# Performance work log

Hardware: AMD Instinct MI355X
Metric: run time of the kernel (lower is better)

## Reference

```python
import jax, jax.numpy as jnp
import numpy as np

B, N, C = 4, 16384, 512
HEADS = 16
HEADC = C // HEADS
HIDDEN = int(C * 4.0)


def setup_inputs() -> dict:
    key = jax.random.key(0)
    ks = jax.random.split(key, 8)
    s1 = 1.0 / np.sqrt(C)
    s2 = 1.0 / np.sqrt(HIDDEN)
    return {
        "x": jax.random.normal(ks[0], (B, N, C), jnp.float32),
        "mask_matrix": jnp.zeros((1,), jnp.int32),
        "norm1_w": jnp.ones((C,), jnp.float32),
        "norm1_b": jnp.zeros((C,), jnp.float32),
        "kln_w": jnp.ones((HEADS, 1, HEADC), jnp.float32),
        "kln_b": jnp.zeros((HEADS, 1, HEADC), jnp.float32),
        "vln_w": jnp.ones((HEADS, 1, HEADC), jnp.float32),
        "vln_b": jnp.zeros((HEADS, 1, HEADC), jnp.float32),
        "norm2_w": jnp.ones((C,), jnp.float32),
        "norm2_b": jnp.zeros((C,), jnp.float32),
        "fc1_w": jax.random.uniform(ks[1], (HIDDEN, C), jnp.float32, -s1, s1),
        "fc1_b": jax.random.uniform(ks[2], (HIDDEN,), jnp.float32, -s1, s1),
        "fc2_w": jax.random.uniform(ks[3], (C, HIDDEN), jnp.float32, -s2, s2),
        "fc2_b": jax.random.uniform(ks[4], (C,), jnp.float32, -s2, s2),
    }


def _ln(t, w, b, eps=1e-5):
    # standard nn.LayerNorm: biased variance, eps inside sqrt
    mean = t.mean(-1, keepdims=True)
    var = ((t - mean) ** 2).mean(-1, keepdims=True)
    return w * (t - mean) / jnp.sqrt(var + eps) + b


def _ln_std(t, w, b, eps=1e-5):
    # custom LayerNorm: unbiased std (torch.std), eps added to std
    d = t.shape[-1]
    mean = t.mean(-1, keepdims=True)
    var = ((t - mean) ** 2).sum(-1, keepdims=True) / (d - 1)
    return w * ((t - mean) / (jnp.sqrt(var) + eps)) + b


def reference(x, mask_matrix, norm1_w, norm1_b, kln_w, kln_b, vln_w, vln_b,
              norm2_w, norm2_b, fc1_w, fc1_b, fc2_w, fc2_b):
    b, n, c = x.shape
    shortcut = x
    h = _ln(x, norm1_w, norm1_b)
    # simple_attn (softmax-free linear attention)
    qkv = h.reshape(b, n, HEADS, HEADC).transpose(0, 2, 1, 3)  # [B,H,N,D]
    q = qkv
    k = _ln_std(qkv, kln_w, kln_b)
    v = _ln_std(qkv, vln_w, vln_b)
    kv = jnp.einsum('bhnd,bhne->bhde', k, v) / n        # [B,H,D,D]
    attn = jnp.einsum('bhnd,bhde->bhne', q, kv)          # [B,H,N,D]
    attn = attn.transpose(0, 2, 1, 3).reshape(b, n, c)
    h = attn + h                                          # residual inside simple_attn (bias = x post-norm1)
    x = shortcut + h
    # MLP branch
    m = _ln(x, norm2_w, norm2_b)
    m = jax.nn.gelu(m @ fc1_w.T + fc1_b, approximate=False)
    m = m @ fc2_w.T + fc2_b
    return x + m
```

## Files before the change

### kernel.cpp

```cpp
#include <hip/hip_runtime.h>
#include <cstdint>

#define BB 4
#define NN 16384
#define CC 512
#define HH 16
#define DD 32
#define HID 2048
#define MTOT (BB * NN)
#define MCHUNK 16384

typedef __bf16 bf16_t;
typedef __bf16 bf16x8 __attribute__((ext_vector_type(8)));
typedef __bf16 bf16x4 __attribute__((ext_vector_type(4)));
typedef float  f32x4  __attribute__((ext_vector_type(4)));

__device__ __forceinline__ void gload_lds16(const void* g, void* l) {
  auto gp = reinterpret_cast<const __attribute__((address_space(1))) char*>(
      reinterpret_cast<uintptr_t>(g));
  auto lp = reinterpret_cast<__attribute__((address_space(3))) char*>(
      reinterpret_cast<uintptr_t>(l));
  __builtin_amdgcn_global_load_lds(gp, lp, 16, 0, 0);
}

__global__ __launch_bounds__(256) void cvt_bf16_kernel(const float* __restrict__ src,
                                                       bf16_t* __restrict__ dst) {
  const long i = ((long)blockIdx.x * 256 + threadIdx.x) * 4;
  const f32x4 v = *(const f32x4*)(src + i);
  bf16x4 o;
  o[0] = (bf16_t)v[0]; o[1] = (bf16_t)v[1]; o[2] = (bf16_t)v[2]; o[3] = (bf16_t)v[3];
  *(bf16x4*)(dst + i) = o;
}

__global__ __launch_bounds__(256) void norm1_kernel(const float* __restrict__ x,
                                                    const float* __restrict__ w,
                                                    const float* __restrict__ bvec,
                                                    bf16_t* __restrict__ h) {
  const int wv = threadIdx.x >> 6, l = threadIdx.x & 63;
  const long tok = (long)blockIdx.x * 4 + wv;
  const int c0 = l * 8;
  const f32x4 a = *(const f32x4*)(x + tok * CC + c0);
  const f32x4 b = *(const f32x4*)(x + tok * CC + c0 + 4);
  float v[8];
#pragma unroll
  for (int i = 0; i < 4; ++i) { v[i] = a[i]; v[4 + i] = b[i]; }
  float s = 0.f, s2 = 0.f;
#pragma unroll
  for (int i = 0; i < 8; ++i) { s += v[i]; s2 += v[i] * v[i]; }
  for (int off = 32; off; off >>= 1) { s += __shfl_xor(s, off); s2 += __shfl_xor(s2, off); }
  const float mean = s * (1.f / CC);
  const float var  = fmaxf(s2 * (1.f / CC) - mean * mean, 0.f);
  const float rstd = rsqrtf(var + 1e-5f);
  const f32x4 w0 = *(const f32x4*)(w + c0), w1 = *(const f32x4*)(w + c0 + 4);
  const f32x4 b0 = *(const f32x4*)(bvec + c0), b1 = *(const f32x4*)(bvec + c0 + 4);
  bf16x8 o;
#pragma unroll
  for (int i = 0; i < 4; ++i) {
    o[i]     = (bf16_t)(w0[i] * (v[i] - mean) * rstd + b0[i]);
    o[4 + i] = (bf16_t)(w1[i] * (v[4 + i] - mean) * rstd + b1[i]);
  }
  *(bf16x8*)(h + tok * CC + c0) = o;
}

__global__ __launch_bounds__(256) void kv_partial_kernel(const bf16_t* __restrict__ h,
                                                         const float* __restrict__ klw,
                                                         const float* __restrict__ klb,
                                                         const float* __restrict__ vlw,
                                                         const float* __restrict__ vlb,
                                                         float* __restrict__ kvp) {
  __shared__ bf16_t kb[256 * 32];
  __shared__ bf16_t vb[256 * 32];
  __shared__ float scratch[192 * 16];
  const int tid = threadIdx.x;
  const int bh = blockIdx.x >> 6, chunk = blockIdx.x & 63;
  const int head = bh & 15;
  const int b = bh >> 4;
  const long tok0 = ((long)b << 14) + chunk * 256;
  const bf16_t* src = h + (tok0 + tid) * (long)CC + head * DD;
  float hv[32];
  {
    float s = 0.f, s2 = 0.f;
#pragma unroll
    for (int c = 0; c < 4; ++c) {
      const bf16x8 r = *(const bf16x8*)(src + c * 8);
#pragma unroll
      for (int j = 0; j < 8; ++j) {
        hv[c * 8 + j] = (float)r[j]; s += hv[c * 8 + j]; s2 += hv[c * 8 + j] * hv[c * 8 + j];
      }
    }
    const float mean = s * (1.f / 32.f);
    const float varu = fmaxf((s2 - 32.f * mean * mean) * (1.f / 31.f), 0.f);
    const float inv = 1.f / (sqrtf(varu) + 1e-5f);
    const int sx = (tid >> 1) & 3;
#pragma unroll
    for (int c = 0; c < 4; ++c) {
      bf16x8 kc, vc;
#pragma unroll
      for (int j = 0; j < 8; ++j) {
        const int d = c * 8 + j;
        const float t = (hv[d] - mean) * inv;
        kc[j] = (bf16_t)(klw[head * DD + d] * t + klb[head * DD + d]);
        vc[j] = (bf16_t)(vlw[head * DD + d] * t + vlb[head * DD + d]);
      }
      *(bf16x8*)((char*)kb + tid * 64 + ((c ^ sx) * 16)) = kc;
      *(bf16x8*)((char*)vb + tid * 64 + ((c ^ sx) * 16)) = vc;
    }
  }
  __syncthreads();
  const int g = tid >> 6, l = tid & 63;
  const int d0 = (l >> 3) * 4, e0 = (l & 7) * 4;
  const int ck = (l >> 3) >> 1, hk = (l >> 3) & 1;
  const int ce = (l & 7) >> 1, he = l & 1;
  float a[4][4] = {};
  for (int t = g; t < 256; t += 4) {
    const int tx = (t >> 1) & 3;
    const bf16x4 kq = *(const bf16x4*)((const char*)kb + t * 64 + ((ck ^ tx) * 16) + hk * 8);
    const bf16x4 vq = *(const bf16x4*)((const char*)vb + t * 64 + ((ce ^ tx) * 16) + he * 8);
    float kf[4], vf[4];
#pragma unroll
    for (int i2 = 0; i2 < 4; ++i2) { kf[i2] = (float)kq[i2]; vf[i2] = (float)vq[i2]; }
#pragma unroll
    for (int i2 = 0; i2 < 4; ++i2)
#pragma unroll
      for (int j2 = 0; j2 < 4; ++j2) a[i2][j2] += kf[i2] * vf[j2];
  }
  __syncthreads();
  if (g) {
#pragma unroll
    for (int i2 = 0; i2 < 4; ++i2)
#pragma unroll
      for (int j2 = 0; j2 < 4; ++j2)
        scratch[((g - 1) * 64 + l) * 16 + i2 * 4 + j2] = a[i2][j2];
  }
  __syncthreads();
  if (!g) {
#pragma unroll
    for (int gg = 0; gg < 3; ++gg)
#pragma unroll
      for (int i2 = 0; i2 < 4; ++i2)
#pragma unroll
        for (int j2 = 0; j2 < 4; ++j2)
          a[i2][j2] += scratch[(gg * 64 + l) * 16 + i2 * 4 + j2];
    float* dst = kvp + ((long)(bh * 64 + chunk) << 10);
#pragma unroll
    for (int i2 = 0; i2 < 4; ++i2) {
      f32x4 st;
      st[0] = a[i2][0]; st[1] = a[i2][1]; st[2] = a[i2][2]; st[3] = a[i2][3];
      *(f32x4*)&dst[(d0 + i2) * 32 + e0] = st;
    }
  }
}

__global__ __launch_bounds__(256) void kv_reduce_kernel(const float* __restrict__ kvp,
                                                        bf16_t* __restrict__ kvT) {
  const int bh = blockIdx.x;
  const int i4 = threadIdx.x * 4;
  const int d = i4 >> 5, e0 = i4 & 31;
  float s[4] = {};
  const float* p = kvp + ((long)bh << 16) + i4;
  for (int ch = 0; ch < 64; ++ch) {
    const f32x4 t = *(const f32x4*)(p + (ch << 10));
    s[0] += t[0]; s[1] += t[1]; s[2] += t[2]; s[3] += t[3];
  }
  const float sc = 1.f / (float)NN;
  bf16_t* q = kvT + ((long)bh << 10);
#pragma unroll
  for (int j = 0; j < 4; ++j) q[(e0 + j) * 32 + d] = (bf16_t)(s[j] * sc);
}

#define ASTRIDE 520
__global__ __launch_bounds__(256) void attn_fused_kernel(const float* __restrict__ x,
                                                         const bf16_t* __restrict__ h,
                                                         const bf16_t* __restrict__ kvTg,
                                                         const float* __restrict__ n2w,
                                                         const float* __restrict__ n2b,
                                                         float* __restrict__ xout,
                                                         bf16_t* __restrict__ mout) {
  __shared__ bf16_t attn_s[32 * ASTRIDE];
  const int tid = threadIdx.x;
  const int wv = tid >> 6, lane = tid & 63;
  const int lr = lane & 15, kg = lane >> 4;
  const long tok0 = (long)blockIdx.x * 32;
  const int b = (int)(tok0 >> 14);
  const bf16_t* kvsrc = kvTg + ((long)b << 14);

  {
    const int tt = wv & 1, hh = wv >> 1;
    const bf16_t* arow = h + (tok0 + tt * 16 + lr) * (long)CC + kg * 8;
    const f32x4 zero = {};
#pragma unroll
    for (int hi = 0; hi < 8; ++hi) {
      const int hd = hh * 8 + hi;
      const bf16_t* kvh = kvsrc + (hd << 10) + kg * 8;
      const bf16x8 af = *(const bf16x8*)(arow + hd * DD);
      const bf16x8 b0 = *(const bf16x8*)(kvh + lr * 32);
      const bf16x8 b1 = *(const bf16x8*)(kvh + (16 + lr) * 32);
      const f32x4 a0 = __builtin_amdgcn_mfma_f32_16x16x32_bf16(af, b0, zero, 0, 0, 0);
      const f32x4 a1 = __builtin_amdgcn_mfma_f32_16x16x32_bf16(af, b1, zero, 0, 0, 0);
      const int rbase = tt * 16 + kg * 4;
#pragma unroll
      for (int rg = 0; rg < 4; ++rg) {
        attn_s[(rbase + rg) * ASTRIDE + hd * 32 + lr]      = (bf16_t)a0[rg];
        attn_s[(rbase + rg) * ASTRIDE + hd * 32 + 16 + lr] = (bf16_t)a1[rg];
      }
    }
  }
  __syncthreads();

  const int c0 = lane * 8;
  const f32x4 w0 = *(const f32x4*)(n2w + c0), w1 = *(const f32x4*)(n2w + c0 + 4);
  const f32x4 bb0 = *(const f32x4*)(n2b + c0), bb1 = *(const f32x4*)(n2b + c0 + 4);
  for (int it = 0; it < 8; ++it) {
    const int tl = wv * 8 + it;
    const long tok = tok0 + tl;
    const f32x4 xa = *(const f32x4*)(x + tok * CC + c0);
    const f32x4 xb = *(const f32x4*)(x + tok * CC + c0 + 4);
    const bf16x8 hv = *(const bf16x8*)(h + tok * CC + c0);
    const bf16x8 av = *(const bf16x8*)&attn_s[tl * ASTRIDE + c0];
    float x2[8];
#pragma unroll
    for (int i = 0; i < 4; ++i) {
      x2[i]     = xa[i] + (float)hv[i]     + (float)av[i];
      x2[4 + i] = xb[i] + (float)hv[4 + i] + (float)av[4 + i];
    }
    float s = 0.f, s2 = 0.f;
#pragma unroll
    for (int i = 0; i < 8; ++i) { s += x2[i]; s2 += x2[i] * x2[i]; }
    for (int off = 32; off; off >>= 1) { s += __shfl_xor(s, off); s2 += __shfl_xor(s2, off); }
    const float mean = s * (1.f / CC);
    const float var  = fmaxf(s2 * (1.f / CC) - mean * mean, 0.f);
    const float rstd = rsqrtf(var + 1e-5f);
    f32x4 oa, ob;
    bf16x8 om;
#pragma unroll
    for (int i = 0; i < 4; ++i) {
      oa[i] = x2[i]; ob[i] = x2[4 + i];
      om[i]     = (bf16_t)(w0[i] * (x2[i] - mean) * rstd + bb0[i]);
      om[4 + i] = (bf16_t)(w1[i] * (x2[4 + i] - mean) * rstd + bb1[i]);
    }
    *(f32x4*)(xout + tok * CC + c0) = oa;
    *(f32x4*)(xout + tok * CC + c0 + 4) = ob;
    *(bf16x8*)(mout + tok * CC + c0) = om;
  }
}

template <int K, int NOUT, int BN, int WMC, int WNC, bool GELU>
__global__ __launch_bounds__(512, 2) void gemm_kernel(const bf16_t* __restrict__ A,
                                                      const bf16_t* __restrict__ Bw,
                                                      const float* __restrict__ bias,
                                                      bf16_t* __restrict__ outb,
                                                      float* __restrict__ outf) {
  constexpr int ABYTES = 256 * 64;
  constexpr int BBYTES = BN * 64;
  constexpr int BUFB = ABYTES + BBYTES;
  constexpr int LOADS = BUFB / 8192;
  constexpr int MREP = 256 / WMC / 16;
  constexpr int NREP = BN / WNC / 16;
  constexpr int NTILE = NOUT / BN;
  constexpr int NT = K / 32;

  __shared__ bf16_t lds[3 * BUFB / 2];
  const int tid = threadIdx.x;
  const int wid = tid >> 6, lane = tid & 63;
  const int wm = wid / WNC, wn = wid % WNC;
  const int lr = lane & 15, kg = lane >> 4;

  int bid = blockIdx.x;
  const int q = gridDim.x >> 3;
  bid = (bid & 7) * q + (bid >> 3);
  const int bx = bid % NTILE;
  const long by = bid / NTILE;
  const long row0 = by * 256;
  const long col0 = (long)bx * BN;

  const int srow = tid >> 2;
  const int swc = ((tid & 3) ^ ((srow >> 1) & 3)) * 8;
  const bf16_t* gA = A + (row0 + srow) * (long)K + swc;
  const bf16_t* gB = Bw + (col0 + srow) * (long)K + swc;
  char* ldsb = (char*)lds;

#define STAGEK(bufi, kt) do {                                            \
    char* base_ = ldsb + (bufi) * BUFB;                                  \
    gload_lds16(gA + (kt) * 32,            base_ + tid * 16);            \
    gload_lds16(gA + 128L * K + (kt) * 32, base_ + 8192 + tid * 16);     \
    gload_lds16(gB + (kt) * 32,            base_ + ABYTES + tid * 16);   \
    if constexpr (BN == 256)                                             \
      gload_lds16(gB + 128L * K + (kt) * 32,                             \
                  base_ + ABYTES + 8192 + tid * 16);                     \
  } while (0)

  f32x4 acc[MREP][NREP] = {};

  STAGEK(0, 0);
  STAGEK(1, 1);
  if constexpr (LOADS == 4) asm volatile("s_waitcnt vmcnt(4)" ::: "memory");
  else                      asm volatile("s_waitcnt vmcnt(3)" ::: "memory");
  __builtin_amdgcn_s_barrier();

  for (int t = 0; t < NT; ++t) {
    const int cur = t % 3;
    if (t + 2 < NT) STAGEK((t + 2) % 3, t + 2);
    const char* ab = (const char*)ldsb + cur * BUFB;
    const char* bb = ab + ABYTES;
    bf16x8 af[MREP], bf[NREP];
#pragma unroll
    for (int m = 0; m < MREP; ++m) {
      const int row = wm * (256 / WMC) + m * 16 + lr;
      af[m] = *(const bf16x8*)(ab + row * 64 + ((kg ^ ((row >> 1) & 3)) * 16));
    }
#pragma unroll
    for (int n = 0; n < NREP; ++n) {
      const int row = wn * (BN / WNC) + n * 16 + lr;
      bf[n] = *(const bf16x8*)(bb + row * 64 + ((kg ^ ((row >> 1) & 3)) * 16));
    }
    __builtin_amdgcn_s_setprio(1);
#pragma unroll
    for (int m = 0; m < MREP; ++m)
#pragma unroll
      for (int n = 0; n < NREP; ++n)
        acc[m][n] = __builtin_amdgcn_mfma_f32_16x16x32_bf16(af[m], bf[n], acc[m][n], 0, 0, 0);
    __builtin_amdgcn_s_setprio(0);
    if (t + 1 < NT) {
      if (t + 2 < NT) {
        if constexpr (LOADS == 4) asm volatile("s_waitcnt vmcnt(4)" ::: "memory");
        else                      asm volatile("s_waitcnt vmcnt(3)" ::: "memory");
      } else {
        asm volatile("s_waitcnt vmcnt(0)" ::: "memory");
      }
      __builtin_amdgcn_s_barrier();
    }
  }
#undef STAGEK

#pragma unroll
  for (int n = 0; n < NREP; ++n) {
    const long col = col0 + wn * (BN / WNC) + n * 16 + lr;
    const float bs = bias[col];
#pragma unroll
    for (int m = 0; m < MREP; ++m) {
#pragma unroll
      for (int rg = 0; rg < 4; ++rg) {
        const long row = row0 + wm * (256 / WMC) + m * 16 + kg * 4 + rg;
        const float v = acc[m][n][rg] + bs;
        if constexpr (GELU) {
          const float u = 0.7978845608028654f * (v + 0.044715f * v * v * v);
          const float gv = v / (1.f + __expf(-2.f * u));
          outb[row * NOUT + col] = (bf16_t)gv;
        } else {
          outf[row * NOUT + col] += v;
        }
      }
    }
  }
}

extern "C" void kernel_launch(void* const* d_in, const int* in_sizes, int n_in,
                              void* d_out, int out_size, void* d_ws, size_t ws_size,
                              hipStream_t stream) {
  const float* x   = (const float*)d_in[0];
  const float* n1w = (const float*)d_in[2];
  const float* n1b = (const float*)d_in[3];
  const float* klw = (const float*)d_in[4];
  const float* klb = (const float*)d_in[5];
  const float* vlw = (const float*)d_in[6];
  const float* vlb = (const float*)d_in[7];
  const float* n2w = (const float*)d_in[8];
  const float* n2b = (const float*)d_in[9];
  const float* w1f = (const float*)d_in[10];
  const float* b1  = (const float*)d_in[11];
  const float* w2f = (const float*)d_in[12];
  const float* b2  = (const float*)d_in[13];
  float* out = (float*)d_out;

  char* ws = (char*)d_ws;
  bf16_t* h   = (bf16_t*)(ws);
  bf16_t* mb  = (bf16_t*)(ws + (size_t)67108864);
  bf16_t* act = (bf16_t*)(ws + (size_t)134217728);
  bf16_t* w1  = (bf16_t*)(ws + (size_t)201326592);
  bf16_t* w2  = (bf16_t*)(ws + (size_t)203423744);
  float*  kvp = (float*)(ws + (size_t)205520896);
  bf16_t* kvT = (bf16_t*)(ws + (size_t)222298112);

  cvt_bf16_kernel<<<1024, 256, 0, stream>>>(w1f, w1);
  cvt_bf16_kernel<<<1024, 256, 0, stream>>>(w2f, w2);
  norm1_kernel<<<MTOT / 4, 256, 0, stream>>>(x, n1w, n1b, h);
  kv_partial_kernel<<<BB * HH * 64, 256, 0, stream>>>(h, klw, klb, vlw, vlb, kvp);
  kv_reduce_kernel<<<BB * HH, 256, 0, stream>>>(kvp, kvT);
  attn_fused_kernel<<<MTOT / 32, 256, 0, stream>>>(x, h, kvT, n2w, n2b, out, mb);
  for (int ch = 0; ch < MTOT / MCHUNK; ++ch) {
    gemm_kernel<CC, HID, 256, 2, 4, true>
        <<<(MCHUNK / 256) * (HID / 256), 512, 0, stream>>>(
        mb + (long)ch * MCHUNK * CC, w1, b1, act, nullptr);
    gemm_kernel<HID, CC, 128, 4, 2, false>
        <<<(MCHUNK / 256) * (CC / 128), 512, 0, stream>>>(
        act, w2, b2, nullptr, out + (long)ch * MCHUNK * CC);
  }
}
```

Baseline: 633.6 us.

## Rewrite MLP GEMMs as 8-phase ping-pong pipeline with 64-wide K tiles

```diff
diff --git a/kernel.cpp b/kernel.cpp
--- a/kernel.cpp
+++ b/kernel.cpp
@@ -244,104 +244,133 @@
   }
 }
 
-template <int K, int NOUT, int BN, int WMC, int WNC, bool GELU>
-__global__ __launch_bounds__(512, 2) void gemm_kernel(const bf16_t* __restrict__ A,
-                                                      const bf16_t* __restrict__ Bw,
-                                                      const float* __restrict__ bias,
-                                                      bf16_t* __restrict__ outb,
-                                                      float* __restrict__ outf) {
-  constexpr int ABYTES = 256 * 64;
-  constexpr int BBYTES = BN * 64;
-  constexpr int BUFB = ABYTES + BBYTES;
-  constexpr int LOADS = BUFB / 8192;
-  constexpr int MREP = 256 / WMC / 16;
-  constexpr int NREP = BN / WNC / 16;
+template <int K, int NOUT, int BN, bool GELU>
+__global__ __launch_bounds__(512, 2) void gemm8p_kernel(const bf16_t* __restrict__ A,
+                                                        const bf16_t* __restrict__ Bw,
+                                                        const float* __restrict__ bias,
+                                                        bf16_t* __restrict__ outb,
+                                                        float* __restrict__ outf) {
   constexpr int NTILE = NOUT / BN;
-  constexpr int NT = K / 32;
-
-  __shared__ bf16_t lds[3 * BUFB / 2];
+  constexpr int NT = K / 64;
+  constexpr int NI = NT / 2;
+  constexpr int WNSPAN = BN / 4;
+  constexpr int NH = WNSPAN / 32;
+  constexpr int NREP = 2 * NH;
+  constexpr int BLOADS = BN / 128;
+  constexpr int ABYT = 32768;
+  constexpr int BBYT = BN * 128;
+  constexpr int BUFB = ABYT + BBYT;
+  constexpr int WVM = 2 + BLOADS;
+
+  __shared__ char lds[2 * BUFB];
+
   const int tid = threadIdx.x;
   const int wid = tid >> 6, lane = tid & 63;
-  const int wm = wid / WNC, wn = wid % WNC;
+  const int wm = wid >> 2, wn = wid & 3;
   const int lr = lane & 15, kg = lane >> 4;
 
   int bid = blockIdx.x;
-  const int q = gridDim.x >> 3;
-  bid = (bid & 7) * q + (bid >> 3);
-  const int bx = bid % NTILE;
-  const long by = bid / NTILE;
-  const long row0 = by * 256;
-  const long col0 = (long)bx * BN;
+  const int qq = gridDim.x >> 3;
+  bid = (bid & 7) * qq + (bid >> 3);
+  const long row0 = (long)(bid / NTILE) * 256;
+  const long col0 = (long)(bid % NTILE) * BN;
 
   const int srow = tid >> 2;
-  const int swc = ((tid & 3) ^ ((srow >> 1) & 3)) * 8;
-  const bf16_t* gA = A + (row0 + srow) * (long)K + swc;
-  const bf16_t* gB = Bw + (col0 + srow) * (long)K + swc;
-  char* ldsb = (char*)lds;
-
-#define STAGEK(bufi, kt) do {                                            \
-    char* base_ = ldsb + (bufi) * BUFB;                                  \
-    gload_lds16(gA + (kt) * 32,            base_ + tid * 16);            \
-    gload_lds16(gA + 128L * K + (kt) * 32, base_ + 8192 + tid * 16);     \
-    gload_lds16(gB + (kt) * 32,            base_ + ABYTES + tid * 16);   \
-    if constexpr (BN == 256)                                             \
-      gload_lds16(gB + 128L * K + (kt) * 32,                             \
-                  base_ + ABYTES + 8192 + tid * 16);                     \
-  } while (0)
-
-  f32x4 acc[MREP][NREP] = {};
-
-  STAGEK(0, 0);
-  STAGEK(1, 1);
-  if constexpr (LOADS == 4) asm volatile("s_waitcnt vmcnt(4)" ::: "memory");
-  else                      asm volatile("s_waitcnt vmcnt(3)" ::: "memory");
-  __builtin_amdgcn_s_barrier();
-
-  for (int t = 0; t < NT; ++t) {
-    const int cur = t % 3;
-    if (t + 2 < NT) STAGEK((t + 2) % 3, t + 2);
-    const char* ab = (const char*)ldsb + cur * BUFB;
-    const char* bb = ab + ABYTES;
-    bf16x8 af[MREP], bf[NREP];
-#pragma unroll
-    for (int m = 0; m < MREP; ++m) {
-      const int row = wm * (256 / WMC) + m * 16 + lr;
-      af[m] = *(const bf16x8*)(ab + row * 64 + ((kg ^ ((row >> 1) & 3)) * 16));
-    }
-#pragma unroll
-    for (int n = 0; n < NREP; ++n) {
-      const int row = wn * (BN / WNC) + n * 16 + lr;
-      bf[n] = *(const bf16x8*)(bb + row * 64 + ((kg ^ ((row >> 1) & 3)) * 16));
-    }
+  const int sce = (((tid & 3) ^ ((srow >> 1) & 3)) << 3);
+  const bf16_t* pA = A + (row0 + srow) * (long)K + sce;
+  const bf16_t* pB = Bw + (col0 + srow) * (long)K + sce;
+  char* ldsp = (char*)lds;
+
+  auto SA = [&](int buf, int ks, int kt) {
+    char* d_ = ldsp + buf * BUFB + ks * 16384 + tid * 16;
+    const bf16_t* g_ = pA + (long)kt * 64 + ks * 32;
+    gload_lds16(g_, d_);
+    gload_lds16(g_ + 128L * K, d_ + 8192);
+  };
+  auto SB = [&](int buf, int ks, int kt) {
+    char* d_ = ldsp + buf * BUFB + ABYT + ks * (BN * 64) + tid * 16;
+    const bf16_t* g_ = pB + (long)kt * 64 + ks * 32;
+    gload_lds16(g_, d_);
+    if constexpr (BLOADS == 2) gload_lds16(g_ + 128L * K, d_ + 8192);
+  };
+
+  f32x4 acc[8][NREP] = {};
+  bf16x8 af[8], bf[NH];
+
+  auto LDA8 = [&](int buf, int ks) {
+    const char* b_ = ldsp + buf * BUFB + ks * 16384;
+#pragma unroll
+    for (int m = 0; m < 8; ++m) {
+      const int row = wm * 128 + m * 16 + lr;
+      af[m] = *(const bf16x8*)(b_ + row * 64 + ((kg ^ ((row >> 1) & 3)) << 4));
+    }
+  };
+  auto LDBN = [&](int buf, int ks, int nh) {
+    const char* b_ = ldsp + buf * BUFB + ABYT + ks * (BN * 64);
+#pragma unroll
+    for (int n = 0; n < NH; ++n) {
+      const int row = wn * WNSPAN + nh * (WNSPAN / 2) + n * 16 + lr;
+      bf[n] = *(const bf16x8*)(b_ + row * 64 + ((kg ^ ((row >> 1) & 3)) << 4));
+    }
+  };
+  auto MM = [&](int nh) {
     __builtin_amdgcn_s_setprio(1);
 #pragma unroll
-    for (int m = 0; m < MREP; ++m)
-#pragma unroll
-      for (int n = 0; n < NREP; ++n)
-        acc[m][n] = __builtin_amdgcn_mfma_f32_16x16x32_bf16(af[m], bf[n], acc[m][n], 0, 0, 0);
+    for (int m = 0; m < 8; ++m)
+#pragma unroll
+      for (int n = 0; n < NH; ++n)
+        acc[m][nh * NH + n] =
+            __builtin_amdgcn_mfma_f32_16x16x32_bf16(af[m], bf[n], acc[m][nh * NH + n], 0, 0, 0);
     __builtin_amdgcn_s_setprio(0);
-    if (t + 1 < NT) {
-      if (t + 2 < NT) {
-        if constexpr (LOADS == 4) asm volatile("s_waitcnt vmcnt(4)" ::: "memory");
-        else                      asm volatile("s_waitcnt vmcnt(3)" ::: "memory");
-      } else {
-        asm volatile("s_waitcnt vmcnt(0)" ::: "memory");
-      }
-      __builtin_amdgcn_s_barrier();
-    }
-  }
-#undef STAGEK
-
-#pragma unroll
-  for (int n = 0; n < NREP; ++n) {
-    const long col = col0 + wn * (BN / WNC) + n * 16 + lr;
+  };
+  auto WVMW = [&]() {
+    if constexpr (WVM == 4) asm volatile("s_waitcnt vmcnt(4)" ::: "memory");
+    else                    asm volatile("s_waitcnt vmcnt(3)" ::: "memory");
+  };
+#define BARX() __builtin_amdgcn_s_barrier()
+#define LGKM0() asm volatile("s_waitcnt lgkmcnt(0)" ::: "memory")
+
+  SA(0, 0, 0); SA(0, 1, 0); SB(0, 0, 0); SB(0, 1, 0);
+  SA(1, 0, 1); SB(1, 0, 1);
+  WVMW();
+  BARX();
+
+  for (int i = 0; i < NI; ++i) {
+    const int t1 = 2 * i + 1, tA = 2 * i + 2, tB = 2 * i + 3;
+    const bool last = (i == NI - 1);
+    LDA8(0, 0); LDBN(0, 0, 0); SA(1, 1, t1);
+    BARX(); LGKM0(); MM(0); BARX();
+    LDBN(0, 0, 1); SB(1, 1, t1);
+    BARX(); LGKM0(); MM(1); BARX();
+    LDA8(0, 1); LDBN(0, 1, 0); if (tA < NT) SA(0, 0, tA);
+    BARX(); LGKM0(); MM(0); BARX();
+    LDBN(0, 1, 1); if (tA < NT) SB(0, 0, tA);
+    BARX(); LGKM0(); MM(1);
+    if (last) asm volatile("s_waitcnt vmcnt(0)" ::: "memory"); else WVMW();
+    BARX();
+    LDA8(1, 0); LDBN(1, 0, 0); if (tA < NT) SA(0, 1, tA);
+    BARX(); LGKM0(); MM(0); BARX();
+    LDBN(1, 0, 1); if (tA < NT) SB(0, 1, tA);
+    BARX(); LGKM0(); MM(1); BARX();
+    LDA8(1, 1); LDBN(1, 1, 0); if (tB < NT) SA(1, 0, tB);
+    BARX(); LGKM0(); MM(0); BARX();
+    LDBN(1, 1, 1); if (tB < NT) SB(1, 0, tB);
+    BARX(); LGKM0(); MM(1);
+    if (!last) { WVMW(); BARX(); }
+  }
+#undef BARX
+#undef LGKM0
+
+#pragma unroll
+  for (int j = 0; j < NREP; ++j) {
+    const long col = col0 + wn * WNSPAN + j * 16 + lr;
     const float bs = bias[col];
 #pragma unroll
-    for (int m = 0; m < MREP; ++m) {
+    for (int m = 0; m < 8; ++m) {
 #pragma unroll
       for (int rg = 0; rg < 4; ++rg) {
-        const long row = row0 + wm * (256 / WMC) + m * 16 + kg * 4 + rg;
-        const float v = acc[m][n][rg] + bs;
+        const long row = row0 + wm * 128 + m * 16 + kg * 4 + rg;
+        const float v = acc[m][j][rg] + bs;
         if constexpr (GELU) {
           const float u = 0.7978845608028654f * (v + 0.044715f * v * v * v);
           const float gv = v / (1.f + __expf(-2.f * u));
@@ -388,10 +417,10 @@
   kv_reduce_kernel<<<BB * HH, 256, 0, stream>>>(kvp, kvT);
   attn_fused_kernel<<<MTOT / 32, 256, 0, stream>>>(x, h, kvT, n2w, n2b, out, mb);
   for (int ch = 0; ch < MTOT / MCHUNK; ++ch) {
-    gemm_kernel<CC, HID, 256, 2, 4, true>
+    gemm8p_kernel<CC, HID, 256, true>
         <<<(MCHUNK / 256) * (HID / 256), 512, 0, stream>>>(
         mb + (long)ch * MCHUNK * CC, w1, b1, act, nullptr);
-    gemm_kernel<HID, CC, 128, 4, 2, false>
+    gemm8p_kernel<HID, CC, 128, false>
         <<<(MCHUNK / 256) * (CC / 128), 512, 0, stream>>>(
         act, w2, b2, nullptr, out + (long)ch * MCHUNK * CC);
   }
```

Result: no change. 638.9 us (+0.8%).

## Replace triple-buffered 256-row GEMM with simple 128x128 single-buffer tiles and LDS-staged GELU stores

Applied to the files above, without the earlier changes.

```diff
diff --git a/kernel.cpp b/kernel.cpp
--- a/kernel.cpp
+++ b/kernel.cpp
@@ -8,7 +8,6 @@
 #define DD 32
 #define HID 2048
 #define MTOT (BB * NN)
-#define MCHUNK 16384
 
 typedef __bf16 bf16_t;
 typedef __bf16 bf16x8 __attribute__((ext_vector_type(8)));
@@ -244,110 +243,98 @@
   }
 }
 
-template <int K, int NOUT, int BN, int WMC, int WNC, bool GELU>
-__global__ __launch_bounds__(512, 2) void gemm_kernel(const bf16_t* __restrict__ A,
-                                                      const bf16_t* __restrict__ Bw,
-                                                      const float* __restrict__ bias,
-                                                      bf16_t* __restrict__ outb,
-                                                      float* __restrict__ outf) {
-  constexpr int ABYTES = 256 * 64;
-  constexpr int BBYTES = BN * 64;
-  constexpr int BUFB = ABYTES + BBYTES;
-  constexpr int LOADS = BUFB / 8192;
-  constexpr int MREP = 256 / WMC / 16;
-  constexpr int NREP = BN / WNC / 16;
-  constexpr int NTILE = NOUT / BN;
+template <int K, int NOUT, bool GELU>
+__global__ __launch_bounds__(256, 3) void gemm97_kernel(const bf16_t* __restrict__ A,
+                                                        const bf16_t* __restrict__ Bw,
+                                                        const float* __restrict__ bias,
+                                                        bf16_t* __restrict__ outb,
+                                                        float* __restrict__ outf) {
+  constexpr int NTILE = NOUT / 128;
   constexpr int NT = K / 32;
-
-  __shared__ bf16_t lds[3 * BUFB / 2];
+  __shared__ char lds[32768];
+  char* As = lds;
+  char* Bs = lds + 8192;
+
   const int tid = threadIdx.x;
   const int wid = tid >> 6, lane = tid & 63;
-  const int wm = wid / WNC, wn = wid % WNC;
+  const int wr = wid >> 1, wc = wid & 1;
   const int lr = lane & 15, kg = lane >> 4;
 
   int bid = blockIdx.x;
-  const int q = gridDim.x >> 3;
-  bid = (bid & 7) * q + (bid >> 3);
-  const int bx = bid % NTILE;
-  const long by = bid / NTILE;
-  const long row0 = by * 256;
-  const long col0 = (long)bx * BN;
+  const int qq = gridDim.x >> 3;
+  bid = (bid & 7) * qq + (bid >> 3);
+  const long row0 = (long)(bid / NTILE) * 128;
+  const long col0 = (long)(bid % NTILE) * 128;
 
   const int srow = tid >> 2;
-  const int swc = ((tid & 3) ^ ((srow >> 1) & 3)) * 8;
-  const bf16_t* gA = A + (row0 + srow) * (long)K + swc;
-  const bf16_t* gB = Bw + (col0 + srow) * (long)K + swc;
-  char* ldsb = (char*)lds;
-
-#define STAGEK(bufi, kt) do {                                            \
-    char* base_ = ldsb + (bufi) * BUFB;                                  \
-    gload_lds16(gA + (kt) * 32,            base_ + tid * 16);            \
-    gload_lds16(gA + 128L * K + (kt) * 32, base_ + 8192 + tid * 16);     \
-    gload_lds16(gB + (kt) * 32,            base_ + ABYTES + tid * 16);   \
-    if constexpr (BN == 256)                                             \
-      gload_lds16(gB + 128L * K + (kt) * 32,                             \
-                  base_ + ABYTES + 8192 + tid * 16);                     \
-  } while (0)
-
-  f32x4 acc[MREP][NREP] = {};
-
-  STAGEK(0, 0);
-  STAGEK(1, 1);
-  if constexpr (LOADS == 4) asm volatile("s_waitcnt vmcnt(4)" ::: "memory");
-  else                      asm volatile("s_waitcnt vmcnt(3)" ::: "memory");
-  __builtin_amdgcn_s_barrier();
-
-  for (int t = 0; t < NT; ++t) {
-    const int cur = t % 3;
-    if (t + 2 < NT) STAGEK((t + 2) % 3, t + 2);
-    const char* ab = (const char*)ldsb + cur * BUFB;
-    const char* bb = ab + ABYTES;
-    bf16x8 af[MREP], bf[NREP];
-#pragma unroll
-    for (int m = 0; m < MREP; ++m) {
-      const int row = wm * (256 / WMC) + m * 16 + lr;
-      af[m] = *(const bf16x8*)(ab + row * 64 + ((kg ^ ((row >> 1) & 3)) * 16));
-    }
-#pragma unroll
-    for (int n = 0; n < NREP; ++n) {
-      const int row = wn * (BN / WNC) + n * 16 + lr;
-      bf[n] = *(const bf16x8*)(bb + row * 64 + ((kg ^ ((row >> 1) & 3)) * 16));
-    }
-    __builtin_amdgcn_s_setprio(1);
-#pragma unroll
-    for (int m = 0; m < MREP; ++m)
-#pragma unroll
-      for (int n = 0; n < NREP; ++n)
+  const int sce = (((tid & 3) ^ ((srow >> 1) & 3)) << 3);
+  const bf16_t* gA = A + (row0 + srow) * (long)K + sce;
+  const bf16_t* gB = Bw + (col0 + srow) * (long)K + sce;
+
+  f32x4 acc[4][4] = {};
+
+  const int cx = ((kg ^ ((lr >> 1) & 3)) << 4);
+  const char* aB = As + (wr * 64 + lr) * 64 + cx;
+  const char* bB = Bs + (wc * 64 + lr) * 64 + cx;
+
+  for (int kt = 0; kt < NT; ++kt) {
+    gload_lds16(gA + kt * 32, As + tid * 16);
+    gload_lds16(gA + 64L * K + kt * 32, As + 4096 + tid * 16);
+    gload_lds16(gB + kt * 32, Bs + tid * 16);
+    gload_lds16(gB + 64L * K + kt * 32, Bs + 4096 + tid * 16);
+    __syncthreads();
+    bf16x8 af[4], bf[4];
+#pragma unroll
+    for (int m = 0; m < 4; ++m) af[m] = *(const bf16x8*)(aB + m * 1024);
+#pragma unroll
+    for (int n = 0; n < 4; ++n) bf[n] = *(const bf16x8*)(bB + n * 1024);
+#pragma unroll
+    for (int m = 0; m < 4; ++m)
+#pragma unroll
+      for (int n = 0; n < 4; ++n)
         acc[m][n] = __builtin_amdgcn_mfma_f32_16x16x32_bf16(af[m], bf[n], acc[m][n], 0, 0, 0);
-    __builtin_amdgcn_s_setprio(0);
-    if (t + 1 < NT) {
-      if (t + 2 < NT) {
-        if constexpr (LOADS == 4) asm volatile("s_waitcnt vmcnt(4)" ::: "memory");
-        else                      asm volatile("s_waitcnt vmcnt(3)" ::: "memory");
-      } else {
-        asm volatile("s_waitcnt vmcnt(0)" ::: "memory");
-      }
-      __builtin_amdgcn_s_barrier();
-    }
-  }
-#undef STAGEK
-
-#pragma unroll
-  for (int n = 0; n < NREP; ++n) {
-    const long col = col0 + wn * (BN / WNC) + n * 16 + lr;
-    const float bs = bias[col];
-#pragma unroll
-    for (int m = 0; m < MREP; ++m) {
-#pragma unroll
-      for (int rg = 0; rg < 4; ++rg) {
-        const long row = row0 + wm * (256 / WMC) + m * 16 + kg * 4 + rg;
-        const float v = acc[m][n][rg] + bs;
-        if constexpr (GELU) {
+    __syncthreads();
+  }
+
+  if constexpr (GELU) {
+    bf16_t* ot = (bf16_t*)lds;
+#pragma unroll
+    for (int n = 0; n < 4; ++n) {
+      const int col = wc * 64 + n * 16 + lr;
+      const float bs = bias[col0 + col];
+#pragma unroll
+      for (int m = 0; m < 4; ++m) {
+#pragma unroll
+        for (int rg = 0; rg < 4; ++rg) {
+          const int row = wr * 64 + m * 16 + kg * 4 + rg;
+          const float v = acc[m][n][rg] + bs;
           const float u = 0.7978845608028654f * (v + 0.044715f * v * v * v);
           const float gv = v / (1.f + __expf(-2.f * u));
-          outb[row * NOUT + col] = (bf16_t)gv;
-        } else {
-          outf[row * NOUT + col] += v;
+          const int ch = (col >> 3) ^ ((row >> 2) & 3);
+          ot[row * 128 + ch * 8 + (col & 7)] = (bf16_t)gv;
+        }
+      }
+    }
+    __syncthreads();
+#pragma unroll
+    for (int it2 = 0; it2 < 8; ++it2) {
+      const int idx = it2 * 256 + tid;
+      const int row = idx >> 4, ch = idx & 15;
+      const int chs = ch ^ ((row >> 2) & 3);
+      const bf16x8 vv = *(const bf16x8*)&ot[row * 128 + chs * 8];
+      *(bf16x8*)(outb + (row0 + row) * NOUT + col0 + ch * 8) = vv;
+    }
+  } else {
+#pragma unroll
+    for (int n = 0; n < 4; ++n) {
+      const long col = col0 + wc * 64 + n * 16 + lr;
+      const float bs = bias[col];
+#pragma unroll
+      for (int m = 0; m < 4; ++m) {
+#pragma unroll
+        for (int rg = 0; rg < 4; ++rg) {
+          const long row = row0 + wr * 64 + m * 16 + kg * 4 + rg;
+          outf[row * NOUT + col] += acc[m][n][rg] + bs;
         }
       }
     }
@@ -372,14 +359,20 @@
   const float* b2  = (const float*)d_in[13];
   float* out = (float*)d_out;
 
+  int nch;
+  if (ws_size >= 289538048ULL) nch = 2;
+  else                         nch = 4;
+  const long mch = MTOT / nch;
+
   char* ws = (char*)d_ws;
-  bf16_t* h   = (bf16_t*)(ws);
-  bf16_t* mb  = (bf16_t*)(ws + (size_t)67108864);
-  bf16_t* act = (bf16_t*)(ws + (size_t)134217728);
-  bf16_t* w1  = (bf16_t*)(ws + (size_t)201326592);
-  bf16_t* w2  = (bf16_t*)(ws + (size_t)203423744);
-  float*  kvp = (float*)(ws + (size_t)205520896);
-  bf16_t* kvT = (bf16_t*)(ws + (size_t)222298112);
+  size_t off = 0;
+  bf16_t* h   = (bf16_t*)(ws + off); off += (size_t)MTOT * CC * 2;
+  bf16_t* mb  = (bf16_t*)(ws + off); off += (size_t)MTOT * CC * 2;
+  bf16_t* act = (bf16_t*)(ws + off); off += (size_t)mch * HID * 2;
+  bf16_t* w1  = (bf16_t*)(ws + off); off += (size_t)HID * CC * 2;
+  bf16_t* w2  = (bf16_t*)(ws + off); off += (size_t)HID * CC * 2;
+  float*  kvp = (float*)(ws + off);  off += (size_t)BB * HH * 64 * 1024 * 4;
+  bf16_t* kvT = (bf16_t*)(ws + off);
 
   cvt_bf16_kernel<<<1024, 256, 0, stream>>>(w1f, w1);
   cvt_bf16_kernel<<<1024, 256, 0, stream>>>(w2f, w2);
@@ -387,12 +380,12 @@
   kv_partial_kernel<<<BB * HH * 64, 256, 0, stream>>>(h, klw, klb, vlw, vlb, kvp);
   kv_reduce_kernel<<<BB * HH, 256, 0, stream>>>(kvp, kvT);
   attn_fused_kernel<<<MTOT / 32, 256, 0, stream>>>(x, h, kvT, n2w, n2b, out, mb);
-  for (int ch = 0; ch < MTOT / MCHUNK; ++ch) {
-    gemm_kernel<CC, HID, 256, 2, 4, true>
-        <<<(MCHUNK / 256) * (HID / 256), 512, 0, stream>>>(
-        mb + (long)ch * MCHUNK * CC, w1, b1, act, nullptr);
-    gemm_kernel<HID, CC, 128, 4, 2, false>
-        <<<(MCHUNK / 256) * (CC / 128), 512, 0, stream>>>(
-        act, w2, b2, nullptr, out + (long)ch * MCHUNK * CC);
-  }
-}
+  for (int ch = 0; ch < nch; ++ch) {
+    gemm97_kernel<CC, HID, true>
+        <<<(int)((mch / 128) * (HID / 128)), 256, 0, stream>>>(
+        mb + (size_t)ch * mch * CC, w1, b1, act, nullptr);
+    gemm97_kernel<HID, CC, false>
+        <<<(int)((mch / 128) * (CC / 128)), 256, 0, stream>>>(
+        act, w2, b2, nullptr, out + (size_t)ch * mch * CC);
+  }
+}
```

Measured after the change: 663.0 us. 4.6% more time.
